# Kernel optimization log

Hardware: AMD Instinct MI355X
Metric: run time of the kernel (lower is better)

## Reference

```python
import jax, jax.numpy as jnp
import numpy as np

N_EXPERTS = 8
TOP_K = 2


def setup_inputs() -> dict:
    key = jax.random.key(0)
    k1, k2, k3, k4 = jax.random.split(key, 4)
    B, T, C, H, E = 2, 2048, 1024, 4096, N_EXPERTS
    x = jax.random.normal(k1, (B, T, C), dtype=jnp.float32)
    # weights scaled like standard init to keep activations well-behaved
    router_w = jax.random.normal(k2, (E, C), dtype=jnp.float32) * 0.02
    w1 = jax.random.normal(k3, (E, C, H), dtype=jnp.float32) * (1.0 / np.sqrt(C))
    w2 = jax.random.normal(k4, (E, H, C), dtype=jnp.float32) * (1.0 / np.sqrt(H))
    return {"x": x, "router_w": router_w, "w1": w1, "w2": w2}


def reference(x, router_w, w1, w2):
    B, T, C = x.shape
    E = N_EXPERTS
    xf = x.reshape(-1, C)                                   # [N, C], N = B*T
    logits = jnp.einsum('nc,ec->ne', xf, router_w)          # router (no bias)
    probs = jax.nn.softmax(logits, axis=-1)
    top_w, top_i = jax.lax.top_k(probs, TOP_K)              # [N, K]
    top_w = top_w / jnp.sum(top_w, axis=-1, keepdims=True)  # renormalize
    # combine weight per (token, expert): sum of top-k weights routed to e
    comb = jnp.einsum('nk,nke->ne', top_w, jax.nn.one_hot(top_i, E, dtype=xf.dtype))
    # dense all-expert compute (bias=False, exact GELU, dropout=0 at eval)
    h = jax.nn.gelu(jnp.einsum('nc,ech->enh', xf, w1), approximate=False)  # [E, N, H]
    y = jnp.einsum('enh,ehc->enc', h, w2)                   # [E, N, C]
    out = jnp.einsum('ne,enc->nc', comb, y)                 # weighted combine
    return out.reshape(B, T, C)
```

## Files before the change

### kernel.cpp

```cpp
#include <hip/hip_runtime.h>
#include <hip/hip_bf16.h>
#include <stdint.h>

#define NTOK 4096
#define CD   1024
#define HD   4096
#define NE   8

typedef __attribute__((ext_vector_type(8))) short bf16x8;
typedef __attribute__((ext_vector_type(4))) float f32x4;
typedef __attribute__((ext_vector_type(4))) unsigned short us4;

#define BARR() asm volatile("s_barrier" ::: "memory")
#define VM2() asm volatile("s_waitcnt vmcnt(2)" ::: "memory")
#define VM0() asm volatile("s_waitcnt vmcnt(0)" ::: "memory")

__device__ __forceinline__ unsigned short f2bf(float f){
  __hip_bfloat16 h = __float2bfloat16(f);
  return *reinterpret_cast<unsigned short*>(&h);
}

__global__ __launch_bounds__(256) void router_kernel(
    const float* __restrict__ x, const float* __restrict__ rw,
    unsigned short* __restrict__ x_bf, int* __restrict__ top_i,
    float* __restrict__ top_w, int* __restrict__ counts){
  __shared__ float rw_lds[NE*CD];
  int tid = threadIdx.x;
  for (int i = tid; i < NE*CD/4; i += 256)
    ((float4*)rw_lds)[i] = ((const float4*)rw)[i];
  __syncthreads();
  int l = tid & 63, w = tid >> 6;
  int n = blockIdx.x*4 + w;

  float4 xv[4];
  #pragma unroll
  for (int j = 0; j < 4; ++j)
    xv[j] = ((const float4*)(x + (size_t)n*CD))[l + j*64];

  #pragma unroll
  for (int j = 0; j < 4; ++j){
    us4 o; o.x = f2bf(xv[j].x); o.y = f2bf(xv[j].y); o.z = f2bf(xv[j].z); o.w = f2bf(xv[j].w);
    *(us4*)(x_bf + (size_t)n*CD + l*4 + j*256) = o;
  }

  double le[NE];
  #pragma unroll
  for (int e = 0; e < NE; ++e){
    double p = 0.0;
    #pragma unroll
    for (int j = 0; j < 4; ++j){
      float4 rv = ((const float4*)(rw_lds + e*CD))[l + j*64];
      p += (double)xv[j].x*rv.x + (double)xv[j].y*rv.y + (double)xv[j].z*rv.z + (double)xv[j].w*rv.w;
    }
    #pragma unroll
    for (int d = 32; d >= 1; d >>= 1) p += __shfl_xor(p, d);
    le[e] = p;
  }
  if (l == 0){
    double m = le[0];
    #pragma unroll
    for (int e = 1; e < NE; ++e) m = le[e] > m ? le[e] : m;
    double pe[NE];
    #pragma unroll
    for (int e = 0; e < NE; ++e) pe[e] = exp(le[e]-m);
    int i0 = 0;
    #pragma unroll
    for (int e = 1; e < NE; ++e) if (pe[e] > pe[i0]) i0 = e;
    int i1 = (i0 == 0) ? 1 : 0;
    #pragma unroll
    for (int e = 0; e < NE; ++e){ if (e == i0) continue; if (pe[e] > pe[i1]) i1 = e; }
    double w0 = pe[i0], w1v = pe[i1], wsum = w0 + w1v;
    top_i[2*n] = i0; top_i[2*n+1] = i1;
    top_w[2*n] = (float)(w0/wsum); top_w[2*n+1] = (float)(w1v/wsum);
    atomicAdd(&counts[i0], 1); atomicAdd(&counts[i1], 1);
  }
}

__global__ void scan_kernel(const int* __restrict__ counts, int* __restrict__ offsets, int* __restrict__ cursor){
  if (threadIdx.x == 0){
    int s = 0;
    for (int e = 0; e < NE; ++e){ offsets[e] = s; cursor[e] = s; s += counts[e]; }
  }
}

__global__ __launch_bounds__(256) void scatter_kernel(
    const int* __restrict__ top_i, const float* __restrict__ top_w,
    int* __restrict__ cursor, int* __restrict__ g_tok, float* __restrict__ g_w){
  int n = blockIdx.x*256 + threadIdx.x;
  #pragma unroll
  for (int k = 0; k < 2; ++k){
    int e = top_i[2*n+k];
    int pos = atomicAdd(&cursor[e], 1);
    g_tok[pos] = n;
    g_w[pos] = top_w[2*n+k];
  }
}

template<int R, int S>
__global__ __launch_bounds__(256) void transpose_cvt(const float* __restrict__ in, unsigned short* __restrict__ outp){
  __shared__ float tile[64][65];
  int e = blockIdx.z;
  const float* ip = in + (size_t)e*R*S;
  unsigned short* op = outp + (size_t)e*R*S;
  int s0 = blockIdx.x*64, r0 = blockIdx.y*64;
  int tid = threadIdx.x;
  #pragma unroll
  for (int i = 0; i < 4; ++i){
    int lin = i*256 + tid;
    int rr = lin >> 4, c4 = lin & 15;
    float4 v = *(const float4*)(ip + (size_t)(r0+rr)*S + s0 + c4*4);
    tile[rr][c4*4+0] = v.x; tile[rr][c4*4+1] = v.y;
    tile[rr][c4*4+2] = v.z; tile[rr][c4*4+3] = v.w;
  }
  __syncthreads();
  #pragma unroll
  for (int i = 0; i < 4; ++i){
    int lin = i*256 + tid;
    int ss = lin >> 4, rq = lin & 15;
    us4 o;
    o.x = f2bf(tile[rq*4+0][ss]);
    o.y = f2bf(tile[rq*4+1][ss]);
    o.z = f2bf(tile[rq*4+2][ss]);
    o.w = f2bf(tile[rq*4+3][ss]);
    *(us4*)(op + (size_t)(s0+ss)*R + r0 + rq*4) = o;
  }
}

template<int KLEN, int SPLITK, int EPI>
__global__ __launch_bounds__(512, 6) void gemm_ring3(
    const unsigned short* __restrict__ A_src,
    const unsigned short* __restrict__ B_src,
    unsigned short* __restrict__ h_out,
    float* __restrict__ outp,
    const int* __restrict__ g_tok,
    const float* __restrict__ g_w,
    const int* __restrict__ counts,
    const int* __restrict__ offsets,
    int NDIM, int KSTRIDE){
  constexpr int NT = KLEN/32;
  __shared__ alignas(128) char lds[49152];

  int GN = gridDim.x, GY = gridDim.y;
  int p  = blockIdx.x + GN*(blockIdx.y + GY*blockIdx.z);
  int k8 = p & 7, qq = p >> 3;
  int t  = qq / GY, y = qq % GY;
  int j  = k8 + 8*t;
  int xb = j % GN, z = j / GN;

  int e  = (SPLITK == 1) ? z : (z / SPLITK);
  int kz = (SPLITK == 1) ? 0 : (z % SPLITK);
  int n_e = counts[e];
  int m0 = y*128;
  if (m0 >= n_e) return;
  int n0 = xb*128;
  int g_base = offsets[e];
  int kstart = kz*KLEN;

  int tid = threadIdx.x, l = tid & 63, w = tid >> 6;
  int wr = w >> 2, wc = w & 3;
  int lrow = l & 15, q = l >> 4;

  const unsigned short* src[2];
  uint32_t dst[2];
  #pragma unroll
  for (int i = 0; i < 2; ++i){
    int g = i*512 + tid;
    bool isA = g < 512;
    int gg = isA ? g : (g - 512);
    int row = gg >> 2, c = gg & 3;
    int cs = c ^ (row & 3);
    if (isA){
      int rg = m0 + row; if (rg > n_e-1) rg = n_e-1;
      size_t arow;
      if (EPI == 0) arow = (size_t)g_tok[g_base + rg];
      else          arow = (size_t)(g_base + rg);
      src[i] = A_src + arow*(size_t)KSTRIDE + kstart + cs*8;
    } else {
      src[i] = B_src + ((size_t)e*NDIM + n0 + row)*(size_t)KSTRIDE + kstart + cs*8;
    }
    dst[i] = (uint32_t)g*16u;
  }

  auto STAGE = [&](int tt, uint32_t bufoff){
    #pragma unroll
    for (int i = 0; i < 2; ++i)
      __builtin_amdgcn_global_load_lds(
        (const __attribute__((address_space(1))) void*)(src[i] + (size_t)tt*32),
        (__attribute__((address_space(3))) void*)&lds[dst[i] + bufoff], 16, 0, 0);
  };

  uint32_t a_off[4], b_off[2];
  #pragma unroll
  for (int m = 0; m < 4; ++m){
    int ra = wr*64 + m*16 + lrow;
    a_off[m] = (uint32_t)(ra*64) + 16u*(q ^ (ra & 3));
  }
  #pragma unroll
  for (int n = 0; n < 2; ++n){
    int rb = wc*32 + n*16 + lrow;
    b_off[n] = 8192u + (uint32_t)(rb*64) + 16u*(q ^ (rb & 3));
  }

  f32x4 acc[4][2] = {};

  STAGE(0, 0u); STAGE(1, 16384u);

  uint32_t ro = 0u;
  uint32_t so = 32768u;
  #pragma unroll 1
  for (int kt = 0; kt < NT; ++kt){
    if (kt < NT-1) { VM2(); } else { VM0(); }
    BARR();
    if (kt + 2 < NT) STAGE(kt + 2, so);
    bf16x8 av[4], bv[2];
    #pragma unroll
    for (int m = 0; m < 4; ++m)
      av[m] = *(const bf16x8*)&lds[a_off[m] + ro];
    #pragma unroll
    for (int n = 0; n < 2; ++n)
      bv[n] = *(const bf16x8*)&lds[b_off[n] + ro];
    __builtin_amdgcn_s_setprio(1);
    #pragma unroll
    for (int m = 0; m < 4; ++m)
      #pragma unroll
      for (int n = 0; n < 2; ++n)
        acc[m][n] = __builtin_amdgcn_mfma_f32_16x16x32_bf16(av[m], bv[n], acc[m][n], 0, 0, 0);
    __builtin_amdgcn_s_setprio(0);
    ro = (ro == 32768u) ? 0u : ro + 16384u;
    so = (so == 32768u) ? 0u : so + 16384u;
  }

  if (EPI == 0){
    #pragma unroll
    for (int m = 0; m < 4; ++m){
      #pragma unroll
      for (int jj = 0; jj < 4; ++jj){
        int r = m0 + wr*64 + m*16 + q*4 + jj;
        if (r < n_e){
          unsigned short* hp = h_out + (size_t)(g_base + r)*NDIM + n0 + wc*32 + lrow;
          #pragma unroll
          for (int n = 0; n < 2; ++n){
            float v = acc[m][n][jj];
            v = 0.5f*v*(1.0f + erff(v*0.70710678118654752f));
            hp[n*16] = f2bf(v);
          }
        }
      }
    }
  } else {
    #pragma unroll
    for (int m = 0; m < 4; ++m){
      #pragma unroll
      for (int jj = 0; jj < 4; ++jj){
        int r = m0 + wr*64 + m*16 + q*4 + jj;
        if (r < n_e){
          int slot = g_base + r;
          int tt = g_tok[slot];
          float wgt = g_w[slot];
          float* op = outp + (size_t)tt*NDIM + n0 + wc*32 + lrow;
          #pragma unroll
          for (int n = 0; n < 2; ++n)
            atomicAdd(op + n*16, wgt*acc[m][n][jj]);
        }
      }
    }
  }
}

extern "C" void kernel_launch(void* const* d_in, const int* in_sizes, int n_in,
                              void* d_out, int out_size, void* d_ws, size_t ws_size,
                              hipStream_t stream) {
  const float* x  = (const float*)d_in[0];
  const float* rw = (const float*)d_in[1];
  const float* w1 = (const float*)d_in[2];
  const float* w2 = (const float*)d_in[3];

  size_t off = 0;
  auto alloc = [&](size_t sz) -> char* {
    char* p = (char*)d_ws + off;
    off += (sz + 255) & ~(size_t)255;
    return p;
  };
  unsigned short* x_bf = (unsigned short*)alloc((size_t)NTOK*CD*2);
  unsigned short* w1t  = (unsigned short*)alloc((size_t)NE*CD*HD*2);
  unsigned short* w2t  = (unsigned short*)alloc((size_t)NE*CD*HD*2);
  unsigned short* hbuf = (unsigned short*)alloc((size_t)NTOK*2*HD*2);
  int*   top_i  = (int*)alloc(NTOK*2*4);
  float* top_w  = (float*)alloc(NTOK*2*4);
  int*   counts = (int*)alloc(64);
  int*   offs   = (int*)alloc(64);
  int*   cursor = (int*)alloc(64);
  int*   g_tok  = (int*)alloc(NTOK*2*4);
  float* g_w    = (float*)alloc(NTOK*2*4);
  (void)ws_size; (void)in_sizes; (void)n_in; (void)out_size;

  hipMemsetAsync(d_out, 0, (size_t)NTOK*CD*4, stream);
  hipMemsetAsync(counts, 0, 64, stream);

  router_kernel<<<dim3(NTOK/4), dim3(256), 0, stream>>>(x, rw, x_bf, top_i, top_w, counts);
  scan_kernel<<<dim3(1), dim3(64), 0, stream>>>(counts, offs, cursor);
  scatter_kernel<<<dim3(NTOK/256), dim3(256), 0, stream>>>(top_i, top_w, cursor, g_tok, g_w);

  transpose_cvt<CD, HD><<<dim3(HD/64, CD/64, NE), dim3(256), 0, stream>>>(w1, w1t);
  transpose_cvt<HD, CD><<<dim3(CD/64, HD/64, NE), dim3(256), 0, stream>>>(w2, w2t);

  gemm_ring3<CD, 1, 0><<<dim3(HD/128, 12, NE), dim3(512), 0, stream>>>(
      x_bf, w1t, hbuf, (float*)nullptr, g_tok, g_w, counts, offs, HD, CD);
  gemm_ring3<HD/4, 4, 1><<<dim3(CD/128, 12, NE*4), dim3(512), 0, stream>>>(
      hbuf, w2t, (unsigned short*)nullptr, (float*)d_out, g_tok, g_w, counts, offs, CD, HD);
}
```

Measured before the change: 485.0 us.

## Remap GEMM block order to pin expert slices per XCD and halve split-K

```diff
diff --git a/kernel.cpp b/kernel.cpp
--- a/kernel.cpp
+++ b/kernel.cpp
@@ -138,14 +138,18 @@
     const int* __restrict__ offsets,
     int NDIM, int KSTRIDE){
   constexpr int NT = KLEN/32;
+  constexpr int ZPX = (NE*SPLITK)/8;
   __shared__ alignas(128) char lds[49152];
 
   int GN = gridDim.x, GY = gridDim.y;
   int p  = blockIdx.x + GN*(blockIdx.y + GY*blockIdx.z);
-  int k8 = p & 7, qq = p >> 3;
-  int t  = qq / GY, y = qq % GY;
-  int j  = k8 + 8*t;
-  int xb = j % GN, z = j / GN;
+  int k8 = p & 7;
+  int i  = p >> 3;
+  int s  = i / (GN*GY);
+  int r  = i - s*(GN*GY);
+  int y  = r % GY;
+  int xb = r / GY;
+  int z  = k8*ZPX + s;
 
   int e  = (SPLITK == 1) ? z : (z / SPLITK);
   int kz = (SPLITK == 1) ? 0 : (z % SPLITK);
@@ -163,8 +167,8 @@
   const unsigned short* src[2];
   uint32_t dst[2];
   #pragma unroll
-  for (int i = 0; i < 2; ++i){
-    int g = i*512 + tid;
+  for (int ii = 0; ii < 2; ++ii){
+    int g = ii*512 + tid;
     bool isA = g < 512;
     int gg = isA ? g : (g - 512);
     int row = gg >> 2, c = gg & 3;
@@ -174,19 +178,19 @@
       size_t arow;
       if (EPI == 0) arow = (size_t)g_tok[g_base + rg];
       else          arow = (size_t)(g_base + rg);
-      src[i] = A_src + arow*(size_t)KSTRIDE + kstart + cs*8;
+      src[ii] = A_src + arow*(size_t)KSTRIDE + kstart + cs*8;
     } else {
-      src[i] = B_src + ((size_t)e*NDIM + n0 + row)*(size_t)KSTRIDE + kstart + cs*8;
+      src[ii] = B_src + ((size_t)e*NDIM + n0 + row)*(size_t)KSTRIDE + kstart + cs*8;
     }
-    dst[i] = (uint32_t)g*16u;
+    dst[ii] = (uint32_t)g*16u;
   }
 
   auto STAGE = [&](int tt, uint32_t bufoff){
     #pragma unroll
-    for (int i = 0; i < 2; ++i)
+    for (int ii = 0; ii < 2; ++ii)
       __builtin_amdgcn_global_load_lds(
-        (const __attribute__((address_space(1))) void*)(src[i] + (size_t)tt*32),
-        (__attribute__((address_space(3))) void*)&lds[dst[i] + bufoff], 16, 0, 0);
+        (const __attribute__((address_space(1))) void*)(src[ii] + (size_t)tt*32),
+        (__attribute__((address_space(3))) void*)&lds[dst[ii] + bufoff], 16, 0, 0);
   };
 
   uint32_t a_off[4], b_off[2];
@@ -235,9 +239,9 @@
     for (int m = 0; m < 4; ++m){
       #pragma unroll
       for (int jj = 0; jj < 4; ++jj){
-        int r = m0 + wr*64 + m*16 + q*4 + jj;
-        if (r < n_e){
-          unsigned short* hp = h_out + (size_t)(g_base + r)*NDIM + n0 + wc*32 + lrow;
+        int rr = m0 + wr*64 + m*16 + q*4 + jj;
+        if (rr < n_e){
+          unsigned short* hp = h_out + (size_t)(g_base + rr)*NDIM + n0 + wc*32 + lrow;
           #pragma unroll
           for (int n = 0; n < 2; ++n){
             float v = acc[m][n][jj];
@@ -252,9 +256,9 @@
     for (int m = 0; m < 4; ++m){
       #pragma unroll
       for (int jj = 0; jj < 4; ++jj){
-        int r = m0 + wr*64 + m*16 + q*4 + jj;
-        if (r < n_e){
-          int slot = g_base + r;
+        int rr = m0 + wr*64 + m*16 + q*4 + jj;
+        if (rr < n_e){
+          int slot = g_base + rr;
           int tt = g_tok[slot];
           float wgt = g_w[slot];
           float* op = outp + (size_t)tt*NDIM + n0 + wc*32 + lrow;
@@ -306,6 +310,6 @@
 
   gemm_ring3<CD, 1, 0><<<dim3(HD/128, 12, NE), dim3(512), 0, stream>>>(
       x_bf, w1t, hbuf, (float*)nullptr, g_tok, g_w, counts, offs, HD, CD);
-  gemm_ring3<HD/4, 4, 1><<<dim3(CD/128, 12, NE*4), dim3(512), 0, stream>>>(
+  gemm_ring3<HD/2, 2, 1><<<dim3(CD/128, 12, NE*2), dim3(512), 0, stream>>>(
       hbuf, w2t, (unsigned short*)nullptr, (float*)d_out, g_tok, g_w, counts, offs, CD, HD);
 }
```

Result: faster. 465.2 us (-4.1%).
